# Kernel optimization log

Hardware: AMD Instinct MI355X
Metric: run time of the kernel (lower is better)

Reference implementation:

```python
import jax, jax.numpy as jnp
import numpy as np

GROUPS = 32
EPS = 1e-6


def group_norm(x, gamma, beta):
    B, C, H, W = x.shape
    xg = x.reshape(B, GROUPS, C // GROUPS, H, W)
    mu = xg.mean(axis=(2, 3, 4), keepdims=True)
    var = xg.var(axis=(2, 3, 4), keepdims=True)
    xn = ((xg - mu) / jnp.sqrt(var + EPS)).reshape(B, C, H, W)
    return xn * gamma[None, :, None, None] + beta[None, :, None, None]


def conv1x1(h, w, b):
    # 1x1 conv == channel matmul at every pixel
    return jnp.einsum('bchw,oc->bohw', h, w) + b[None, :, None, None]


def setup_inputs() -> dict:
    key = jax.random.key(0)
    ks = jax.random.split(key, 6)
    B, C, H, W = 2, 512, 64, 64
    s = 1.0 / np.sqrt(C)  # kaiming-ish scale for 1x1 conv weights
    return {
        'x': jax.random.normal(ks[0], (B, C, H, W), jnp.float32),
        'gn_gamma': jnp.ones((C,), jnp.float32),
        'gn_beta': jnp.zeros((C,), jnp.float32),
        'wq': jax.random.normal(ks[1], (C, C), jnp.float32) * s,
        'bq': jnp.zeros((C,), jnp.float32),
        'wk': jax.random.normal(ks[2], (C, C), jnp.float32) * s,
        'bk': jnp.zeros((C,), jnp.float32),
        'wv': jax.random.normal(ks[3], (C, C), jnp.float32) * s,
        'bv': jnp.zeros((C,), jnp.float32),
        'wp': jax.random.normal(ks[4], (C, C), jnp.float32) * s,
        'bp': jnp.zeros((C,), jnp.float32),
    }


def reference(x, gn_gamma, gn_beta, wq, bq, wk, bk, wv, bv, wp, bp):
    h = group_norm(x, gn_gamma, gn_beta)
    q = conv1x1(h, wq, bq)
    k = conv1x1(h, wk, bk)
    v = conv1x1(h, wv, bv)
    B, C, H, W = q.shape
    N = H * W
    qf = q.reshape(B, C, N)
    kf = k.reshape(B, C, N)
    vf = v.reshape(B, C, N)
    # scores[b,i,j] = sum_c q[b,c,i] * k[b,c,j], scaled by 1/sqrt(C)
    scores = jnp.einsum('bci,bcj->bij', qf, kf) * (C ** -0.5)
    attn = jax.nn.softmax(scores, axis=2)  # softmax over keys j
    # out[b,c,i] = sum_j v[b,c,j] * attn[b,i,j]
    out = jnp.einsum('bcj,bij->bci', vf, attn).reshape(B, C, H, W)
    out = conv1x1(out, wp, bp)
    return x + out
```

## Files before the change

### kernel.cpp

```cpp
#include <hip/hip_runtime.h>
#include <hip/hip_bf16.h>
#include <math.h>

#define CDIM 512
#define NPIX 4096
#define BATCH 2
#define NGROUP 32
#define CPG 16
#define EPSV 1e-6f

#define QT 64
#define KT 64
#define KS 8
#define KEYS_PER (NPIX / KS)
#define NKT (KEYS_PER / KT)
#define NWIN (NKT * 8)

typedef __attribute__((ext_vector_type(4))) float f32x4;
typedef _Float16 f16x8 __attribute__((ext_vector_type(8)));
typedef __attribute__((ext_vector_type(8))) unsigned short ushort8v;
typedef __attribute__((ext_vector_type(4))) unsigned short ushort4v;

__device__ inline unsigned short f2h(float x) {
  _Float16 h = (_Float16)x;
  return __builtin_bit_cast(unsigned short, h);
}
__device__ inline float h2f(unsigned short u) {
  return (float)__builtin_bit_cast(_Float16, u);
}

__device__ inline void gload_lds16(const void* g, void* l) {
  __builtin_amdgcn_global_load_lds((const __attribute__((address_space(1))) void*)g,
                                   (__attribute__((address_space(3))) void*)l, 16, 0, 0);
}

__global__ __launch_bounds__(1024)
void gn_kernel(const float* __restrict__ x, const float* __restrict__ gamma,
               const float* __restrict__ beta, float* __restrict__ h) {
  const int NE = CPG * NPIX;
  int b = blockIdx.x >> 5;
  int g = blockIdx.x & 31;
  size_t base = ((size_t)b * CDIM + (size_t)g * CPG) * NPIX;
  const float4* xv = (const float4*)(x + base);
  float4* hv = (float4*)(h + base);
  int t = threadIdx.x;
  float s = 0.f, ss = 0.f;
  for (int i = t; i < NE / 4; i += 1024) {
    float4 v = xv[i];
    s += (v.x + v.y) + (v.z + v.w);
    ss += v.x * v.x + v.y * v.y + v.z * v.z + v.w * v.w;
  }
#pragma unroll
  for (int off = 32; off >= 1; off >>= 1) {
    s += __shfl_down(s, off);
    ss += __shfl_down(ss, off);
  }
  __shared__ float redS[16], redQ[16];
  int wid = t >> 6;
  if ((t & 63) == 0) { redS[wid] = s; redQ[wid] = ss; }
  __syncthreads();
  __shared__ float s_mu, s_rs;
  if (t == 0) {
    float S = 0.f, Q = 0.f;
    for (int w = 0; w < 16; ++w) { S += redS[w]; Q += redQ[w]; }
    float mu = S / NE;
    float var = Q / NE - mu * mu;
    s_mu = mu;
    s_rs = rsqrtf(var + EPSV);
  }
  __syncthreads();
  float mu = s_mu, rs = s_rs;
  for (int i = t; i < NE / 4; i += 1024) {
    int c = g * CPG + (i >> 10);
    float ga = gamma[c] * rs;
    float be = beta[c] - mu * ga;
    float4 v = xv[i];
    v.x = v.x * ga + be;
    v.y = v.y * ga + be;
    v.z = v.z * ga + be;
    v.w = v.w * ga + be;
    hv[i] = v;
  }
}

#define BKc 16
#define WPAD 68

template <int MODE>
__global__ __launch_bounds__(256)
void conv1x1_kernel(const float* __restrict__ W, const float* __restrict__ bias,
                    const float* __restrict__ src, const float* __restrict__ resid,
                    float* __restrict__ dst, unsigned short* __restrict__ dsth,
                    unsigned short* __restrict__ dstl) {
  __shared__ __align__(16) float w_lds[BKc][WPAD];
  __shared__ __align__(16) float h_lds[BKc][64];
  __shared__ __align__(16) unsigned short t_lds[64][72];
  int t = threadIdx.x;
  int nBase = blockIdx.x * 64;
  int oBase = blockIdx.y * 64;
  int b = blockIdx.z;
  const float* srcb = src + (size_t)b * CDIM * NPIX;
  float acc[4][4] = {};
  int o0 = 4 * (t >> 4);
  int j0 = 4 * (t & 15);
  for (int c0 = 0; c0 < CDIM; c0 += BKc) {
    __syncthreads();
#pragma unroll
    for (int kk = 0; kk < 4; ++kk) {
      int idx = t + 256 * kk;
      int o_l = idx >> 4, c_l = idx & 15;
      w_lds[c_l][o_l] = W[(size_t)(oBase + o_l) * CDIM + c0 + c_l];
    }
#pragma unroll
    for (int kk = 0; kk < 4; ++kk) {
      int idx = t + 256 * kk;
      int c_l = idx >> 6, j = idx & 63;
      h_lds[c_l][j] = srcb[(size_t)(c0 + c_l) * NPIX + nBase + j];
    }
    __syncthreads();
#pragma unroll
    for (int kk = 0; kk < BKc; ++kk) {
      float4 a = *(const float4*)&w_lds[kk][o0];
      float4 bv = *(const float4*)&h_lds[kk][j0];
      float av[4] = {a.x, a.y, a.z, a.w};
      float bb[4] = {bv.x, bv.y, bv.z, bv.w};
#pragma unroll
      for (int r = 0; r < 4; ++r)
#pragma unroll
        for (int s2 = 0; s2 < 4; ++s2) acc[r][s2] += av[r] * bb[s2];
    }
  }
  if (MODE == 0) {
#pragma unroll
    for (int r = 0; r < 4; ++r) {
      int o = oBase + o0 + r;
      float bi = bias[o];
      size_t off = ((size_t)b * CDIM + o) * NPIX + nBase + j0;
      float4 out;
      out.x = acc[r][0] + bi;
      out.y = acc[r][1] + bi;
      out.z = acc[r][2] + bi;
      out.w = acc[r][3] + bi;
      float4 rv = *(const float4*)(resid + off);
      out.x += rv.x; out.y += rv.y; out.z += rv.z; out.w += rv.w;
      *(float4*)(dst + off) = out;
    }
  } else if (MODE == 2) {
#pragma unroll
    for (int r = 0; r < 4; ++r) {
      int o = oBase + o0 + r;
      float bi = bias[o];
      size_t off = ((size_t)b * CDIM + o) * NPIX + nBase + j0;
      ushort4v hv;
#pragma unroll
      for (int s2 = 0; s2 < 4; ++s2) hv[s2] = f2h(acc[r][s2] + bi);
      *(ushort4v*)(dsth + off) = hv;
    }
  } else {
    float biv[4];
#pragma unroll
    for (int r = 0; r < 4; ++r) biv[r] = bias[oBase + o0 + r];
#pragma unroll
    for (int phase = 0; phase < 2; ++phase) {
      __syncthreads();
#pragma unroll
      for (int r = 0; r < 4; ++r)
#pragma unroll
        for (int s2 = 0; s2 < 4; ++s2) {
          float val = acc[r][s2] + biv[r];
          unsigned short hu = f2h(val);
          t_lds[j0 + s2][o0 + r] = phase == 0 ? hu : f2h(val - h2f(hu));
        }
      __syncthreads();
      unsigned short* dp = phase == 0 ? dsth : dstl;
      int row = t >> 2, seg = t & 3;
      size_t goff = ((size_t)b * NPIX + nBase + row) * CDIM + oBase + seg * 16;
#pragma unroll
      for (int e = 0; e < 2; ++e)
        *(ushort8v*)(dp + goff + 8 * e) = *(ushort8v*)&t_lds[row][seg * 16 + 8 * e];
    }
  }
}

__global__ __launch_bounds__(256, 2)
void attn_kernel(const unsigned short* __restrict__ qt_hi, const unsigned short* __restrict__ qt_lo,
                 const unsigned short* __restrict__ kt_hi, const unsigned short* __restrict__ kt_lo,
                 const unsigned short* __restrict__ vbuf,
                 unsigned short* __restrict__ opart, float* __restrict__ mlbuf) {
  __shared__ __align__(16) unsigned short ktile[3][2][64 * 64];
  __shared__ __align__(16) unsigned short plds[64 * 72];
  __shared__ float flds[64];

  int t = threadIdx.x;
  int lane = t & 63;
  int l15 = lane & 15;
  int hh = lane >> 4;
  int w = t >> 6;
  int bid = blockIdx.x;
  int pair = bid & 15;
  int b = pair >> 3;
  int ks = pair & 7;
  int qtile = bid >> 4;
  int qBase = qtile * QT;

  const unsigned short* qh = qt_hi + ((size_t)b * NPIX + qBase) * CDIM;
  const unsigned short* ql = qt_lo + ((size_t)b * NPIX + qBase) * CDIM;
  const unsigned short* kh = kt_hi + ((size_t)b * NPIX + ks * KEYS_PER) * CDIM;
  const unsigned short* kl = kt_lo + ((size_t)b * NPIX + ks * KEYS_PER) * CDIM;
  const unsigned short* vb = vbuf + (size_t)b * CDIM * NPIX + ks * KEYS_PER;

  const unsigned short* qrow_h = qh + (size_t)(16 * w + l15) * CDIM + 8 * hh;
  const unsigned short* qrow_l = ql + (size_t)(16 * w + l15) * CDIM + 8 * hh;

  f32x4 Oacc[4][8];
#pragma unroll
  for (int rg = 0; rg < 4; ++rg)
#pragma unroll
    for (int cf = 0; cf < 8; ++cf) Oacc[rg][cf] = (f32x4){0.f, 0.f, 0.f, 0.f};
  float mrow[4], lrow[4];
#pragma unroll
  for (int r = 0; r < 4; ++r) { mrow[r] = -1e30f; lrow[r] = 0.f; }

  const float scale = 0.044194173824159216f;

  auto issue = [&](int g) {
    int ch = g & 7;
    int ktof = (g >> 3) * KT;
    int d = g % 3;
#pragma unroll
    for (int j = 0; j < 4; ++j) {
      int idx = w * 4 + j;
      int hl = idx >> 3;
      int sub = idx & 7;
      const unsigned short* src = hl ? kl : kh;
      int key = sub * 8 + (lane >> 3);
      int cb = (lane & 7) ^ ((lane >> 3) & 7);
      gload_lds16(src + (size_t)(ktof + key) * CDIM + ch * 64 + cb * 8,
                  &ktile[d][hl][sub * 512]);
    }
  };

  issue(0);
  issue(1);

  for (int kt = 0; kt < NKT; ++kt) {
    f32x4 Sacc[4];
#pragma unroll
    for (int f = 0; f < 4; ++f) Sacc[f] = (f32x4){0.f, 0.f, 0.f, 0.f};
    for (int ch = 0; ch < 8; ++ch) {
      int g = kt * 8 + ch;
      if (g + 1 < NWIN) {
        asm volatile("s_waitcnt vmcnt(4)" ::: "memory");
      } else {
        asm volatile("s_waitcnt vmcnt(0)" ::: "memory");
      }
      __builtin_amdgcn_s_barrier();
      if (g + 2 < NWIN) issue(g + 2);
      int d = g % 3;
#pragma unroll
      for (int sc = 0; sc < 2; ++sc) {
        int cc = ch * 2 + sc;
        f16x8 qfh_ = *(const f16x8*)(qrow_h + 32 * cc);
        f16x8 qfl_ = *(const f16x8*)(qrow_l + 32 * cc);
        int cbl = sc * 4 + hh;
#pragma unroll
        for (int f = 0; f < 4; ++f) {
          int key = 16 * f + l15;
          int swz = cbl ^ (key & 7);
          f16x8 bh = *(const f16x8*)&ktile[d][0][key * 64 + swz * 8];
          f16x8 bl = *(const f16x8*)&ktile[d][1][key * 64 + swz * 8];
          Sacc[f] = __builtin_amdgcn_mfma_f32_16x16x32_f16(qfh_, bh, Sacc[f], 0, 0, 0);
          Sacc[f] = __builtin_amdgcn_mfma_f32_16x16x32_f16(qfl_, bh, Sacc[f], 0, 0, 0);
          Sacc[f] = __builtin_amdgcn_mfma_f32_16x16x32_f16(qfh_, bl, Sacc[f], 0, 0, 0);
        }
      }
    }
    int ktof = kt * KT;
#pragma unroll
    for (int r = 0; r < 4; ++r) {
      float sv[4];
#pragma unroll
      for (int f = 0; f < 4; ++f) sv[f] = Sacc[f][r] * scale;
      float mx = fmaxf(fmaxf(sv[0], sv[1]), fmaxf(sv[2], sv[3]));
#pragma unroll
      for (int off = 1; off <= 8; off <<= 1) mx = fmaxf(mx, __shfl_xor(mx, off));
      float mn = fmaxf(mrow[r], mx);
      float rs = 0.f;
      int prow = 16 * w + 4 * hh + r;
#pragma unroll
      for (int f = 0; f < 4; ++f) {
        float p = __expf(sv[f] - mn);
        rs += p;
        plds[prow * 72 + 16 * f + l15] = f2h(p);
      }
#pragma unroll
      for (int off = 1; off <= 8; off <<= 1) rs += __shfl_xor(rs, off);
      float fs = __expf(mrow[r] - mn);
      lrow[r] = lrow[r] * fs + rs;
      mrow[r] = mn;
      if (l15 == 0) flds[prow] = fs;
    }
    asm volatile("s_waitcnt lgkmcnt(0)" ::: "memory");
    __builtin_amdgcn_s_barrier();
#pragma unroll
    for (int rg = 0; rg < 4; ++rg) {
      float fr[4];
#pragma unroll
      for (int r = 0; r < 4; ++r) fr[r] = flds[16 * rg + 4 * hh + r];
#pragma unroll
      for (int cf = 0; cf < 8; ++cf)
#pragma unroll
        for (int r = 0; r < 4; ++r) Oacc[rg][cf][r] *= fr[r];
    }
#pragma unroll
    for (int kc = 0; kc < 2; ++kc) {
      f16x8 ap[4];
#pragma unroll
      for (int rg = 0; rg < 4; ++rg)
        ap[rg] = *(const f16x8*)&plds[(16 * rg + l15) * 72 + 32 * kc + 8 * hh];
#pragma unroll
      for (int cf = 0; cf < 8; ++cf) {
        int chan = 128 * w + 16 * cf + l15;
        f16x8 bv = *(const f16x8*)(vb + (size_t)chan * NPIX + ktof + 32 * kc + 8 * hh);
#pragma unroll
        for (int rg = 0; rg < 4; ++rg)
          Oacc[rg][cf] = __builtin_amdgcn_mfma_f32_16x16x32_f16(ap[rg], bv, Oacc[rg][cf], 0, 0, 0);
      }
    }
  }
  unsigned short* ob = opart + (size_t)pair * CDIM * NPIX;
#pragma unroll
  for (int rg = 0; rg < 4; ++rg)
#pragma unroll
    for (int cf = 0; cf < 8; ++cf) {
      int chan = 128 * w + 16 * cf + l15;
      ushort4v pk;
#pragma unroll
      for (int r = 0; r < 4; ++r) pk[r] = f2h(Oacc[rg][cf][r]);
      *(ushort4v*)(ob + (size_t)chan * NPIX + qBase + 16 * rg + 4 * hh) = pk;
    }
  if (l15 == 0) {
    size_t mlb = (size_t)pair * NPIX;
#pragma unroll
    for (int r = 0; r < 4; ++r) {
      int row = 16 * w + 4 * hh + r;
      mlbuf[(mlb + qBase + row) * 2 + 0] = mrow[r];
      mlbuf[(mlb + qBase + row) * 2 + 1] = lrow[r];
    }
  }
}

__global__ __launch_bounds__(256)
void wn_kernel(const float* __restrict__ mlbuf, float* __restrict__ wn) {
  int idx = blockIdx.x * 256 + threadIdx.x;
  int b = idx >> 12;
  int i = idx & (NPIX - 1);
  float m[KS], l[KS], M = -1e30f;
#pragma unroll
  for (int ks = 0; ks < KS; ++ks) {
    size_t p = ((size_t)(b * KS + ks) * NPIX + i) * 2;
    m[ks] = mlbuf[p];
    l[ks] = mlbuf[p + 1];
    M = fmaxf(M, m[ks]);
  }
  float den = 0.f;
#pragma unroll
  for (int ks = 0; ks < KS; ++ks) den += __expf(m[ks] - M) * l[ks];
  float rden = 1.f / den;
#pragma unroll
  for (int ks = 0; ks < KS; ++ks)
    wn[(size_t)(b * KS + ks) * NPIX + i] = __expf(m[ks] - M) * rden;
}

__global__ __launch_bounds__(256)
void combine_kernel(const unsigned short* __restrict__ opart, const float* __restrict__ wn,
                    float* __restrict__ ao) {
  size_t idx = (size_t)blockIdx.x * 256 + threadIdx.x;
  size_t e = idx * 8;
  int i = (int)(e & (NPIX - 1));
  size_t bc = e >> 12;
  int b = (int)(bc >> 9);
  int c = (int)(bc & 511);
  float acc[8] = {};
#pragma unroll
  for (int ks = 0; ks < KS; ++ks) {
    const unsigned short* op = opart + ((size_t)(b * KS + ks) * CDIM + c) * NPIX + i;
    ushort8v ov = *(const ushort8v*)op;
    const float* wp = wn + (size_t)(b * KS + ks) * NPIX + i;
    float4 w0 = *(const float4*)wp;
    float4 w1 = *(const float4*)(wp + 4);
    acc[0] += w0.x * h2f(ov[0]);
    acc[1] += w0.y * h2f(ov[1]);
    acc[2] += w0.z * h2f(ov[2]);
    acc[3] += w0.w * h2f(ov[3]);
    acc[4] += w1.x * h2f(ov[4]);
    acc[5] += w1.y * h2f(ov[5]);
    acc[6] += w1.z * h2f(ov[6]);
    acc[7] += w1.w * h2f(ov[7]);
  }
  float* dst = ao + bc * NPIX + i;
  float4 o0 = {acc[0], acc[1], acc[2], acc[3]};
  float4 o1 = {acc[4], acc[5], acc[6], acc[7]};
  *(float4*)dst = o0;
  *(float4*)(dst + 4) = o1;
}

extern "C" void kernel_launch(void* const* d_in, const int* in_sizes, int n_in,
                              void* d_out, int out_size, void* d_ws, size_t ws_size,
                              hipStream_t stream) {
  const float* x     = (const float*)d_in[0];
  const float* gamma = (const float*)d_in[1];
  const float* beta  = (const float*)d_in[2];
  const float* wq    = (const float*)d_in[3];
  const float* bq    = (const float*)d_in[4];
  const float* wk    = (const float*)d_in[5];
  const float* bk    = (const float*)d_in[6];
  const float* wv    = (const float*)d_in[7];
  const float* bv    = (const float*)d_in[8];
  const float* wp    = (const float*)d_in[9];
  const float* bp    = (const float*)d_in[10];
  float* out = (float*)d_out;

  const size_t per = (size_t)BATCH * CDIM * NPIX;
  char* ws = (char*)d_ws;
  unsigned short* opart = (unsigned short*)ws;
  float* h = (float*)ws;
  unsigned short* qt_hi = (unsigned short*)(ws + (size_t)BATCH * KS * CDIM * NPIX * 2);
  unsigned short* qt_lo = qt_hi + per;
  unsigned short* kt_hi = qt_lo + per;
  unsigned short* kt_lo = kt_hi + per;
  unsigned short* vbuf  = kt_lo + per;
  float* mlbuf = (float*)(vbuf + per);
  float* wn    = mlbuf + (size_t)BATCH * KS * NPIX * 2;
  float* ao    = (float*)qt_hi;

  gn_kernel<<<dim3(BATCH * NGROUP), dim3(1024), 0, stream>>>(x, gamma, beta, h);
  dim3 cgrid(NPIX / 64, CDIM / 64, BATCH);
  conv1x1_kernel<1><<<cgrid, 256, 0, stream>>>(wq, bq, h, nullptr, nullptr, qt_hi, qt_lo);
  conv1x1_kernel<1><<<cgrid, 256, 0, stream>>>(wk, bk, h, nullptr, nullptr, kt_hi, kt_lo);
  conv1x1_kernel<2><<<cgrid, 256, 0, stream>>>(wv, bv, h, nullptr, nullptr, vbuf, nullptr);
  attn_kernel<<<dim3((NPIX / QT) * BATCH * KS), 256, 0, stream>>>(qt_hi, qt_lo, kt_hi, kt_lo,
                                                                  vbuf, opart, mlbuf);
  wn_kernel<<<dim3(BATCH * NPIX / 256), 256, 0, stream>>>(mlbuf, wn);
  combine_kernel<<<dim3((unsigned)(per / 8 / 256)), 256, 0, stream>>>(opart, wn, ao);
  conv1x1_kernel<0><<<cgrid, 256, 0, stream>>>(wp, bp, ao, x, out, nullptr, nullptr);
}
```

Measured before the change: 797.3 us.

## Drop split-fp16 hi/lo Q·K scores, use single fp16 MFMA path

```diff
diff --git a/kernel.cpp b/kernel.cpp
--- a/kernel.cpp
+++ b/kernel.cpp
@@ -14,7 +14,7 @@
 #define KS 8
 #define KEYS_PER (NPIX / KS)
 #define NKT (KEYS_PER / KT)
-#define NWIN (NKT * 8)
+#define NWIN (NKT * 4)
 
 typedef __attribute__((ext_vector_type(4))) float f32x4;
 typedef _Float16 f16x8 __attribute__((ext_vector_type(8)));
@@ -90,8 +90,7 @@
 __global__ __launch_bounds__(256)
 void conv1x1_kernel(const float* __restrict__ W, const float* __restrict__ bias,
                     const float* __restrict__ src, const float* __restrict__ resid,
-                    float* __restrict__ dst, unsigned short* __restrict__ dsth,
-                    unsigned short* __restrict__ dstl) {
+                    float* __restrict__ dst, unsigned short* __restrict__ dsth) {
   __shared__ __align__(16) float w_lds[BKc][WPAD];
   __shared__ __align__(16) float h_lds[BKc][64];
   __shared__ __align__(16) unsigned short t_lds[64][72];
@@ -160,34 +159,26 @@
     float biv[4];
 #pragma unroll
     for (int r = 0; r < 4; ++r) biv[r] = bias[oBase + o0 + r];
-#pragma unroll
-    for (int phase = 0; phase < 2; ++phase) {
-      __syncthreads();
-#pragma unroll
-      for (int r = 0; r < 4; ++r)
-#pragma unroll
-        for (int s2 = 0; s2 < 4; ++s2) {
-          float val = acc[r][s2] + biv[r];
-          unsigned short hu = f2h(val);
-          t_lds[j0 + s2][o0 + r] = phase == 0 ? hu : f2h(val - h2f(hu));
-        }
-      __syncthreads();
-      unsigned short* dp = phase == 0 ? dsth : dstl;
-      int row = t >> 2, seg = t & 3;
-      size_t goff = ((size_t)b * NPIX + nBase + row) * CDIM + oBase + seg * 16;
-#pragma unroll
-      for (int e = 0; e < 2; ++e)
-        *(ushort8v*)(dp + goff + 8 * e) = *(ushort8v*)&t_lds[row][seg * 16 + 8 * e];
-    }
+    __syncthreads();
+#pragma unroll
+    for (int r = 0; r < 4; ++r)
+#pragma unroll
+      for (int s2 = 0; s2 < 4; ++s2)
+        t_lds[j0 + s2][o0 + r] = f2h(acc[r][s2] + biv[r]);
+    __syncthreads();
+    int row = t >> 2, seg = t & 3;
+    size_t goff = ((size_t)b * NPIX + nBase + row) * CDIM + oBase + seg * 16;
+#pragma unroll
+    for (int e = 0; e < 2; ++e)
+      *(ushort8v*)(dsth + goff + 8 * e) = *(ushort8v*)&t_lds[row][seg * 16 + 8 * e];
   }
 }
 
 __global__ __launch_bounds__(256, 2)
-void attn_kernel(const unsigned short* __restrict__ qt_hi, const unsigned short* __restrict__ qt_lo,
-                 const unsigned short* __restrict__ kt_hi, const unsigned short* __restrict__ kt_lo,
+void attn_kernel(const unsigned short* __restrict__ qt, const unsigned short* __restrict__ kt_,
                  const unsigned short* __restrict__ vbuf,
                  unsigned short* __restrict__ opart, float* __restrict__ mlbuf) {
-  __shared__ __align__(16) unsigned short ktile[3][2][64 * 64];
+  __shared__ __align__(16) unsigned short ktile[3][64 * 128];
   __shared__ __align__(16) unsigned short plds[64 * 72];
   __shared__ float flds[64];
 
@@ -203,14 +194,14 @@
   int qtile = bid >> 4;
   int qBase = qtile * QT;
 
-  const unsigned short* qh = qt_hi + ((size_t)b * NPIX + qBase) * CDIM;
-  const unsigned short* ql = qt_lo + ((size_t)b * NPIX + qBase) * CDIM;
-  const unsigned short* kh = kt_hi + ((size_t)b * NPIX + ks * KEYS_PER) * CDIM;
-  const unsigned short* kl = kt_lo + ((size_t)b * NPIX + ks * KEYS_PER) * CDIM;
+  const unsigned short* kb = kt_ + ((size_t)b * NPIX + ks * KEYS_PER) * CDIM;
   const unsigned short* vb = vbuf + (size_t)b * CDIM * NPIX + ks * KEYS_PER;
 
-  const unsigned short* qrow_h = qh + (size_t)(16 * w + l15) * CDIM + 8 * hh;
-  const unsigned short* qrow_l = ql + (size_t)(16 * w + l15) * CDIM + 8 * hh;
+  const unsigned short* qrow =
+      qt + ((size_t)b * NPIX + qBase + 16 * w + l15) * CDIM + 8 * hh;
+  f16x8 qf[16];
+#pragma unroll
+  for (int cc = 0; cc < 16; ++cc) qf[cc] = *(const f16x8*)(qrow + 32 * cc);
 
   f32x4 Oacc[4][8];
 #pragma unroll
@@ -224,19 +215,17 @@
   const float scale = 0.044194173824159216f;
 
   auto issue = [&](int g) {
-    int ch = g & 7;
-    int ktof = (g >> 3) * KT;
+    int ch2 = g & 3;
+    int ktof = (g >> 2) * KT;
     int d = g % 3;
 #pragma unroll
     for (int j = 0; j < 4; ++j) {
       int idx = w * 4 + j;
-      int hl = idx >> 3;
-      int sub = idx & 7;
-      const unsigned short* src = hl ? kl : kh;
-      int key = sub * 8 + (lane >> 3);
-      int cb = (lane & 7) ^ ((lane >> 3) & 7);
-      gload_lds16(src + (size_t)(ktof + key) * CDIM + ch * 64 + cb * 8,
-                  &ktile[d][hl][sub * 512]);
+      int key = idx * 4 + (lane >> 4);
+      int s = lane & 15;
+      int cb = s ^ (key & 15);
+      gload_lds16(kb + (size_t)(ktof + key) * CDIM + ch2 * 128 + cb * 8,
+                  &ktile[d][idx * 512]);
     }
   };
 
@@ -247,8 +236,8 @@
     f32x4 Sacc[4];
 #pragma unroll
     for (int f = 0; f < 4; ++f) Sacc[f] = (f32x4){0.f, 0.f, 0.f, 0.f};
-    for (int ch = 0; ch < 8; ++ch) {
-      int g = kt * 8 + ch;
+    for (int ch2 = 0; ch2 < 4; ++ch2) {
+      int g = kt * 4 + ch2;
       if (g + 1 < NWIN) {
         asm volatile("s_waitcnt vmcnt(4)" ::: "memory");
       } else {
@@ -258,20 +247,14 @@
       if (g + 2 < NWIN) issue(g + 2);
       int d = g % 3;
 #pragma unroll
-      for (int sc = 0; sc < 2; ++sc) {
-        int cc = ch * 2 + sc;
-        f16x8 qfh_ = *(const f16x8*)(qrow_h + 32 * cc);
-        f16x8 qfl_ = *(const f16x8*)(qrow_l + 32 * cc);
+      for (int sc = 0; sc < 4; ++sc) {
+        int cc = ch2 * 4 + sc;
         int cbl = sc * 4 + hh;
 #pragma unroll
         for (int f = 0; f < 4; ++f) {
-          int key = 16 * f + l15;
-          int swz = cbl ^ (key & 7);
-          f16x8 bh = *(const f16x8*)&ktile[d][0][key * 64 + swz * 8];
-          f16x8 bl = *(const f16x8*)&ktile[d][1][key * 64 + swz * 8];
-          Sacc[f] = __builtin_amdgcn_mfma_f32_16x16x32_f16(qfh_, bh, Sacc[f], 0, 0, 0);
-          Sacc[f] = __builtin_amdgcn_mfma_f32_16x16x32_f16(qfl_, bh, Sacc[f], 0, 0, 0);
-          Sacc[f] = __builtin_amdgcn_mfma_f32_16x16x32_f16(qfh_, bl, Sacc[f], 0, 0, 0);
+          int slot = cbl ^ l15;
+          f16x8 bh = *(const f16x8*)&ktile[d][(16 * f + l15) * 128 + slot * 8];
+          Sacc[f] = __builtin_amdgcn_mfma_f32_16x16x32_f16(qf[cc], bh, Sacc[f], 0, 0, 0);
         }
       }
     }
@@ -425,23 +408,20 @@
   char* ws = (char*)d_ws;
   unsigned short* opart = (unsigned short*)ws;
   float* h = (float*)ws;
-  unsigned short* qt_hi = (unsigned short*)(ws + (size_t)BATCH * KS * CDIM * NPIX * 2);
-  unsigned short* qt_lo = qt_hi + per;
-  unsigned short* kt_hi = qt_lo + per;
-  unsigned short* kt_lo = kt_hi + per;
-  unsigned short* vbuf  = kt_lo + per;
+  unsigned short* qbuf = (unsigned short*)(ws + (size_t)BATCH * KS * CDIM * NPIX * 2);
+  unsigned short* kbuf = qbuf + per;
+  unsigned short* vbuf = kbuf + per;
   float* mlbuf = (float*)(vbuf + per);
   float* wn    = mlbuf + (size_t)BATCH * KS * NPIX * 2;
-  float* ao    = (float*)qt_hi;
+  float* ao    = (float*)qbuf;
 
   gn_kernel<<<dim3(BATCH * NGROUP), dim3(1024), 0, stream>>>(x, gamma, beta, h);
   dim3 cgrid(NPIX / 64, CDIM / 64, BATCH);
-  conv1x1_kernel<1><<<cgrid, 256, 0, stream>>>(wq, bq, h, nullptr, nullptr, qt_hi, qt_lo);
-  conv1x1_kernel<1><<<cgrid, 256, 0, stream>>>(wk, bk, h, nullptr, nullptr, kt_hi, kt_lo);
-  conv1x1_kernel<2><<<cgrid, 256, 0, stream>>>(wv, bv, h, nullptr, nullptr, vbuf, nullptr);
-  attn_kernel<<<dim3((NPIX / QT) * BATCH * KS), 256, 0, stream>>>(qt_hi, qt_lo, kt_hi, kt_lo,
-                                                                  vbuf, opart, mlbuf);
+  conv1x1_kernel<1><<<cgrid, 256, 0, stream>>>(wq, bq, h, nullptr, nullptr, qbuf);
+  conv1x1_kernel<1><<<cgrid, 256, 0, stream>>>(wk, bk, h, nullptr, nullptr, kbuf);
+  conv1x1_kernel<2><<<cgrid, 256, 0, stream>>>(wv, bv, h, nullptr, nullptr, vbuf);
+  attn_kernel<<<dim3((NPIX / QT) * BATCH * KS), 256, 0, stream>>>(qbuf, kbuf, vbuf, opart, mlbuf);
   wn_kernel<<<dim3(BATCH * NPIX / 256), 256, 0, stream>>>(mlbuf, wn);
   combine_kernel<<<dim3((unsigned)(per / 8 / 256)), 256, 0, stream>>>(opart, wn, ao);
-  conv1x1_kernel<0><<<cgrid, 256, 0, stream>>>(wp, bp, ao, x, out, nullptr, nullptr);
-}
+  conv1x1_kernel<0><<<cgrid, 256, 0, stream>>>(wp, bp, ao, x, out, nullptr);
+}
```

Result: faster. 676.5 us (-15.2%).
